# Optimization experiments

Hardware: AMD Instinct MI355X
Metric: run time of the kernel (lower is better)

Reference implementation:

```python
import jax, jax.numpy as jnp
import numpy as np


def _normalize(x):
    # channel mean-subtract then channel L2 normalize, as in MIDMs.forward
    x = x - x.mean(axis=1, keepdims=True)
    return x / jnp.linalg.norm(x, axis=1, keepdims=True)


def setup_inputs() -> dict:
    key = jax.random.key(0)
    ks = jax.random.split(key, 6)
    B, C, H, W = 2, 256, 64, 64
    return {
        "trg_out": jax.random.normal(ks[0], (B, C, H, W), jnp.float32),
        "src_out": jax.random.normal(ks[1], (B, C, H, W), jnp.float32),
        "ref_out": jax.random.normal(ks[2], (B, C, H, W), jnp.float32),
        "src_feats": jax.random.normal(ks[3], (B, 4, H, W), jnp.float32),
        "ref_feats": jax.random.normal(ks[4], (B, 4, H, W), jnp.float32),
        "ref_semantics": jax.random.uniform(ks[5], (B, 151, H, W), jnp.float32),
    }


def reference(trg_out, src_out, ref_out, src_feats, ref_feats, ref_semantics):
    B, C, H, W = trg_out.shape
    L = H * W
    # normalized matching features, flattened over spatial positions
    t = _normalize(trg_out).reshape(B, C, L)   # [B, C, Lt]
    s = _normalize(src_out).reshape(B, C, L)   # [B, C, Ls]
    r = _normalize(ref_out).reshape(B, C, L)

    # Correlation.correlation: dense cosine affinity between all position pairs
    corr_src = jnp.einsum("bci,bcj->bij", t, s)  # [B, Lt, Ls]
    corr_ref = jnp.einsum("bci,bcj->bij", t, r)

    # soft_warp: softmax over source positions, attention-weighted gather
    attn_src = jax.nn.softmax(corr_src, axis=-1)
    attn_ref = jax.nn.softmax(corr_ref, axis=-1)

    warped_src_feat = jnp.einsum("bij,bcj->bci", attn_src,
                                 src_feats.reshape(B, -1, L)).reshape(B, -1, H, W)
    warped_ref_feat = jnp.einsum("bij,bcj->bci", attn_ref,
                                 ref_feats.reshape(B, -1, L)).reshape(B, -1, H, W)
    warped_ref_seg = jnp.einsum("bij,bcj->bci", attn_ref,
                                ref_semantics.reshape(B, -1, L)).reshape(B, -1, H, W)
    return warped_src_feat, warped_ref_feat, warped_ref_seg
```

## Files before the change

kernel.cpp:

```cpp
#include <hip/hip_runtime.h>
#include <hip/hip_bf16.h>
#include <cstdint>
#include <cstddef>

typedef unsigned short u16;
typedef __attribute__((ext_vector_type(8))) __bf16 bf16x8;
typedef __attribute__((ext_vector_type(4))) unsigned u32x4;
typedef __attribute__((ext_vector_type(16))) float f32x16;

#define LPOS 4096
#define CDIM 256
#define LDSBUF 13312

#if __has_builtin(__builtin_amdgcn_exp2f)
#define EXP2(x) __builtin_amdgcn_exp2f(x)
#else
#define EXP2(x) exp2f(x)
#endif

#define GLOAD_LDS16(g, l)                                                      \
  __builtin_amdgcn_global_load_lds(                                            \
      (const __attribute__((address_space(1))) void*)(g),                      \
      (__attribute__((address_space(3))) void*)(l), 16, 0, 0)

__device__ __forceinline__ unsigned f2bfbits(float x) {
  union { float f; unsigned u; } v; v.f = x;
  return (v.u + 0x7FFFu + ((v.u >> 16) & 1u)) >> 16;
}
__device__ __forceinline__ unsigned packbf(float a, float b) {
  __hip_bfloat162 h2 = __float22bfloat162_rn(make_float2(a, b));
  return *(unsigned*)&h2;
}

__global__ void norm_fused(const float* __restrict__ t_in,
                           const float* __restrict__ s_in,
                           const float* __restrict__ r_in,
                           u16* __restrict__ qn, u16* __restrict__ ksn,
                           u16* __restrict__ krn) {
  __shared__ float tile[256 * 33];
  __shared__ float sums[256], sqs[256];
  __shared__ float mv[32], ivv[32];
  int idx = blockIdx.x;
  int ab = idx >> 7, lt = idx & 127;
  int arr = ab >> 1, b = ab & 1;
  int l0 = lt * 32;
  const float* inp = (arr == 0 ? t_in : arr == 1 ? s_in : r_in) + (size_t)b * CDIM * LPOS;
  u16* outp = (arr == 0 ? qn : arr == 1 ? ksn : krn) + (size_t)b * LPOS * CDIM;
  float scale = (arr == 0) ? 1.4426950408889634f : 1.0f;
  int t = threadIdx.x;
  int cg = t >> 5, l = t & 31;
  float sum = 0.f, sq = 0.f;
#pragma unroll 8
  for (int cc = 0; cc < 32; ++cc) {
    int c = cg * 32 + cc;
    float v = inp[(size_t)c * LPOS + l0 + l];
    tile[c * 33 + l] = v;
    sum += v; sq += v * v;
  }
  sums[t] = sum; sqs[t] = sq;
  __syncthreads();
  if (t < 32) {
    float s = 0.f, q = 0.f;
#pragma unroll
    for (int g = 0; g < 8; ++g) { s += sums[g * 32 + t]; q += sqs[g * 32 + t]; }
    float mean = s * (1.0f / CDIM);
    float nsq = q - s * s * (1.0f / CDIM);
    mv[t] = mean;
    ivv[t] = rsqrtf(fmaxf(nsq, 1e-20f)) * scale;
  }
  __syncthreads();
  int c2 = t & 127, ph = t >> 7;
#pragma unroll 4
  for (int rr = 0; rr < 16; ++rr) {
    int pos = ph + rr * 2;
    float m = mv[pos], iv = ivv[pos];
    float v0 = (tile[(2 * c2) * 33 + pos] - m) * iv;
    float v1 = (tile[(2 * c2 + 1) * 33 + pos] - m) * iv;
    *(unsigned*)&outp[(size_t)(l0 + pos) * CDIM + 2 * c2] = packbf(v0, v1);
  }
}

__global__ void build_v(const float* __restrict__ sf, const float* __restrict__ rf,
                        const float* __restrict__ sem,
                        u16* __restrict__ vs, u16* __restrict__ vr) {
  int t = blockIdx.x * 256 + threadIdx.x;
  const int NVS = 2 * 32 * 4096;
  if (t < NVS) {
    int b = t >> 17;
    int c = (t >> 12) & 31;
    int j = t & 4095;
    float v = (c < 4) ? sf[((size_t)b * 4 + c) * LPOS + j] : (c == 4 ? 1.0f : 0.0f);
    vs[t] = (u16)f2bfbits(v);
  } else {
    int t2 = t - NVS;
    if (t2 < 2 * 160 * 4096) {
      int b = t2 / (160 * 4096);
      int rr = t2 % (160 * 4096);
      int c = rr >> 12, j = rr & 4095;
      float v = (c < 151) ? sem[((size_t)b * 151 + c) * LPOS + j]
              : (c < 155) ? rf[((size_t)b * 4 + (c - 151)) * LPOS + j]
              : (c == 155) ? 1.0f : 0.0f;
      vr[((size_t)b * 160 + c) * LPOS + j] = (u16)f2bfbits(v);
    }
  }
}

template <int CT>
__device__ __forceinline__ void flash_body(
    const u16* __restrict__ qb, const u16* __restrict__ kb,
    const u16* __restrict__ vb, float* __restrict__ dst,
    u16 (*lds)[LDSBUF], int wave, int lane, int i_wave, int j_base, int iters) {
  int h = lane >> 5, ln = lane & 31;

  bf16x8 qf[16];
  const u16* qrow = qb + (size_t)(i_wave + ln) * CDIM;
#pragma unroll
  for (int kt = 0; kt < 16; ++kt)
    qf[kt] = *(const bf16x8*)(qrow + kt * 16 + h * 8);
#pragma unroll
  for (int kt = 0; kt < 16; ++kt)
    asm volatile("" : "+v"(*(u32x4*)&qf[kt]));

  f32x16 O[CT];
#pragma unroll
  for (int c = 0; c < CT; ++c)
#pragma unroll
    for (int t = 0; t < 16; ++t) O[c][t] = 0.0f;

  auto stage = [&](int j0s, int buf) {
#pragma unroll
    for (int g = 0; g < 4; ++g) {
      int G = wave * 4 + g;
      int j = 2 * G + h;
      GLOAD_LDS16(kb + (size_t)(j0s + j) * CDIM + (ln ^ (j & 7)) * 8,
                  &lds[buf][G * 512]);
    }
    if constexpr (CT == 5) {
#pragma unroll
      for (int g = 0; g < 3; ++g) {
        int s = wave * 3 + g;
        if (s < 10) {
          int f = s * 64 + lane;
          int p = f / 160;
          int c = f - p * 160;
          GLOAD_LDS16(vb + (size_t)c * LPOS + j0s + p * 8,
                      &lds[buf][8192 + s * 512]);
        }
      }
    }
  };

  int kread_base = ln * 256 + 8 * (h ^ (ln & 1));
  int q = (ln >> 1) & 3;
  const u16* ka[4];
#pragma unroll
  for (int m = 0; m < 4; ++m) ka[m] = &lds[0][kread_base + 16 * (m ^ q)];
  const u16* va = &lds[0][8192 + h * 1280 + ln * 8];

  auto iter_body = [&](int jt, int buf) {
    int j0 = j_base + jt * 32;
    int bo = buf * LDSBUF;
    __syncthreads();

    bf16x8 vf[2];
    if constexpr (CT == 1) {
#pragma unroll
      for (int kt2 = 0; kt2 < 2; ++kt2)
        vf[kt2] = *(const bf16x8*)(vb + (size_t)ln * LPOS + j0 + (2 * kt2 + h) * 8);
    }
    if (jt + 1 < iters) stage(j0 + 32, buf ^ 1);
    f32x16 Sa, Sb;
#pragma unroll
    for (int t = 0; t < 16; ++t) { Sa[t] = 0.0f; Sb[t] = 0.0f; }
#pragma unroll
    for (int kt = 0; kt < 16; kt += 2) {
      bf16x8 ka0 = *(const bf16x8*)(ka[kt & 3] + 64 * (kt >> 2) + bo);
      Sa = __builtin_amdgcn_mfma_f32_32x32x16_bf16(ka0, qf[kt], Sa, 0, 0, 0);
      bf16x8 ka1 = *(const bf16x8*)(ka[(kt + 1) & 3] + 64 * ((kt + 1) >> 2) + bo);
      Sb = __builtin_amdgcn_mfma_f32_32x32x16_bf16(ka1, qf[kt + 1], Sb, 0, 0, 0);
    }
    f32x16 S;
#pragma unroll
    for (int t = 0; t < 16; ++t) S[t] = EXP2(Sa[t] + Sb[t]);

    bf16x8 pb[2];
#pragma unroll
    for (int kh = 0; kh < 2; ++kh) {
      unsigned c0 = packbf(S[kh * 8 + 0], S[kh * 8 + 1]);
      unsigned c1 = packbf(S[kh * 8 + 2], S[kh * 8 + 3]);
      unsigned c2 = packbf(S[kh * 8 + 4], S[kh * 8 + 5]);
      unsigned c3 = packbf(S[kh * 8 + 6], S[kh * 8 + 7]);
      unsigned keep0 = h ? c2 : c0, keep1 = h ? c3 : c1;
      unsigned send0 = h ? c0 : c2, send1 = h ? c1 : c3;
      unsigned recv0 = (unsigned)__shfl_xor((int)send0, 32, 64);
      unsigned recv1 = (unsigned)__shfl_xor((int)send1, 32, 64);
      union { unsigned u[4]; bf16x8 v; } tmp;
      tmp.u[0] = h ? recv0 : keep0;
      tmp.u[1] = h ? recv1 : keep1;
      tmp.u[2] = h ? keep0 : recv0;
      tmp.u[3] = h ? keep1 : recv1;
      pb[kh] = tmp.v;
    }

#pragma unroll
    for (int ct = 0; ct < CT; ++ct)
#pragma unroll
      for (int kt2 = 0; kt2 < 2; ++kt2) {
        bf16x8 vax;
        if constexpr (CT == 5)
          vax = *(const bf16x8*)(va + kt2 * 2560 + ct * 256 + bo);
        else
          vax = vf[kt2];
        O[ct] = __builtin_amdgcn_mfma_f32_32x32x16_bf16(vax, pb[kt2], O[ct], 0, 0, 0);
      }
  };

  stage(j_base, 0);
  for (int jt = 0; jt < iters; jt += 2) {
    iter_body(jt, 0);
    iter_body(jt + 1, 1);
  }

#pragma unroll
  for (int ct = 0; ct < CT; ++ct)
#pragma unroll
    for (int t = 0; t < 16; ++t) {
      int c = ct * 32 + (t & 3) + 8 * (t >> 2) + 4 * h;
      dst[(size_t)c * LPOS + i_wave + ln] = O[ct][t];
    }
}

__global__ __launch_bounds__(256, 2) void flash(
    const u16* __restrict__ qn, const u16* __restrict__ ksn, const u16* __restrict__ krn,
    const u16* __restrict__ vs, const u16* __restrict__ vr,
    float* __restrict__ nsrc, float* __restrict__ nref,
    int nch_src, int nch_ref) {
  __shared__ u16 lds[2][LDSBUF];
  int tid = threadIdx.x;
  int wave = tid >> 6, lane = tid & 63;
  int idx = blockIdx.x;
  int third = idx / 3, m = idx - third * 3;
  if (m == 0) {
    int r = third;
    int chunk = r >> 6, b = (r >> 5) & 1, wgi = r & 31;
    int jchunk = LPOS / nch_ref;
    flash_body<5>(qn + (size_t)b * LPOS * CDIM, krn + (size_t)b * LPOS * CDIM,
                  vr + (size_t)b * 160 * LPOS,
                  nref + (size_t)(chunk * 2 + b) * 160 * LPOS,
                  lds, wave, lane, wgi * 128 + wave * 32, chunk * jchunk,
                  jchunk / 32);
  } else {
    int r = idx - third - 1;
    int chunk = r >> 6, b = (r >> 5) & 1, wgi = r & 31;
    int jchunk = LPOS / nch_src;
    flash_body<1>(qn + (size_t)b * LPOS * CDIM, ksn + (size_t)b * LPOS * CDIM,
                  vs + (size_t)b * 32 * LPOS,
                  nsrc + (size_t)(chunk * 2 + b) * 32 * LPOS,
                  lds, wave, lane, wgi * 128 + wave * 32, chunk * jchunk,
                  jchunk / 32);
  }
}

__global__ void finalize(const float* __restrict__ nsrc, const float* __restrict__ nref,
                         float* __restrict__ out, int nch_src, int nch_ref) {
  int t = blockIdx.x * 256 + threadIdx.x;
  if (t >= 1302528) return;
  if (t < 32768) {
    int b = t >> 14, c = (t >> 12) & 3, i = t & 4095;
    float num = 0.f, den = 0.f;
    for (int k = 0; k < nch_src; ++k) {
      const float* base = nsrc + ((size_t)(k * 2 + b) * 32) * LPOS;
      num += base[(size_t)c * LPOS + i];
      den += base[(size_t)4 * LPOS + i];
    }
    out[t] = num / den;
  } else if (t < 65536) {
    int t1 = t - 32768;
    int b = t1 >> 14, c = (t1 >> 12) & 3, i = t1 & 4095;
    float num = 0.f, den = 0.f;
    for (int k = 0; k < nch_ref; ++k) {
      const float* base = nref + ((size_t)(k * 2 + b) * 160) * LPOS;
      num += base[(size_t)(151 + c) * LPOS + i];
      den += base[(size_t)155 * LPOS + i];
    }
    out[t] = num / den;
  } else {
    int t2 = t - 65536;
    int b = t2 / 618496;
    int rr = t2 % 618496;
    int c = rr >> 12, i = rr & 4095;
    float num = 0.f, den = 0.f;
    for (int k = 0; k < nch_ref; ++k) {
      const float* base = nref + ((size_t)(k * 2 + b) * 160) * LPOS;
      num += base[(size_t)c * LPOS + i];
      den += base[(size_t)155 * LPOS + i];
    }
    out[t] = num / den;
  }
}

extern "C" void kernel_launch(void* const* d_in, const int* in_sizes, int n_in,
                              void* d_out, int out_size, void* d_ws, size_t ws_size,
                              hipStream_t stream) {
  const float* trg  = (const float*)d_in[0];
  const float* srcp = (const float*)d_in[1];
  const float* refp = (const float*)d_in[2];
  const float* sfeat = (const float*)d_in[3];
  const float* rfeat = (const float*)d_in[4];
  const float* rsem  = (const float*)d_in[5];
  float* out = (float*)d_out;

  char* ws = (char*)d_ws;
  size_t o = 0;
  auto alloc = [&](size_t bytes) -> char* {
    char* p = ws + o;
    o += (bytes + 255) & ~(size_t)255;
    return p;
  };
  u16* qn  = (u16*)alloc(2ull * LPOS * CDIM * 2);
  u16* ksn = (u16*)alloc(2ull * LPOS * CDIM * 2);
  u16* krn = (u16*)alloc(2ull * LPOS * CDIM * 2);
  u16* vs  = (u16*)alloc(2ull * 32 * LPOS * 2);
  u16* vr  = (u16*)alloc(2ull * 160 * LPOS * 2);

  size_t fixed = o;
  int nch_ref = 8;
  for (;;) {
    size_t need = fixed + 512 +
                  (size_t)(2 * nch_ref) * 2 * 32 * LPOS * 4 +
                  (size_t)nch_ref * 2 * 160 * LPOS * 4;
    if (need <= ws_size || nch_ref == 1) break;
    nch_ref >>= 1;
  }
  int nch_src = 2 * nch_ref;
  float* nsrc = (float*)alloc((size_t)nch_src * 2 * 32 * LPOS * 4);
  float* nref = (float*)alloc((size_t)nch_ref * 2 * 160 * LPOS * 4);

  hipLaunchKernelGGL(norm_fused, dim3(768), dim3(256), 0, stream,
                     trg, srcp, refp, qn, ksn, krn);
  hipLaunchKernelGGL(build_v, dim3(6144), dim3(256), 0, stream,
                     sfeat, rfeat, rsem, vs, vr);
  hipLaunchKernelGGL(flash, dim3(64 * nch_ref * 3), dim3(256), 0, stream,
                     qn, ksn, krn, vs, vr, nsrc, nref, nch_src, nch_ref);
  hipLaunchKernelGGL(finalize, dim3(5088), dim3(256), 0, stream,
                     nsrc, nref, out, nch_src, nch_ref);
}
```

Before: 168.5 us.

## Double key tile per iteration and read V directly from blocked global layout

Each flash iteration now processes 64 key positions instead of 32, staging only K tiles into a larger LDS buffer and reading V fragments straight from global memory. To make those loads contiguous, build_v writes V in a blocked [j/8][channel][8] layout. The src and ref paths now use the same chunk count, interleaved one-to-one in the grid instead of one ref block per two src blocks. This is meant to halve barrier and loop overhead and drop V staging through LDS. The cost is more register pressure, LDS use rising from about 52 KB to 64 KB per block, and possible load imbalance because ref blocks do five times the P·V work of src blocks.

```diff
diff --git a/kernel.cpp b/kernel.cpp
--- a/kernel.cpp
+++ b/kernel.cpp
@@ -5,12 +5,10 @@
 
 typedef unsigned short u16;
 typedef __attribute__((ext_vector_type(8))) __bf16 bf16x8;
-typedef __attribute__((ext_vector_type(4))) unsigned u32x4;
 typedef __attribute__((ext_vector_type(16))) float f32x16;
 
 #define LPOS 4096
 #define CDIM 256
-#define LDSBUF 13312
 
 #if __has_builtin(__builtin_amdgcn_exp2f)
 #define EXP2(x) __builtin_amdgcn_exp2f(x)
@@ -90,7 +88,7 @@
     int c = (t >> 12) & 31;
     int j = t & 4095;
     float v = (c < 4) ? sf[((size_t)b * 4 + c) * LPOS + j] : (c == 4 ? 1.0f : 0.0f);
-    vs[t] = (u16)f2bfbits(v);
+    vs[(((size_t)b * 512 + (j >> 3)) * 32 + c) * 8 + (j & 7)] = (u16)f2bfbits(v);
   } else {
     int t2 = t - NVS;
     if (t2 < 2 * 160 * 4096) {
@@ -100,7 +98,7 @@
       float v = (c < 151) ? sem[((size_t)b * 151 + c) * LPOS + j]
               : (c < 155) ? rf[((size_t)b * 4 + (c - 151)) * LPOS + j]
               : (c == 155) ? 1.0f : 0.0f;
-      vr[((size_t)b * 160 + c) * LPOS + j] = (u16)f2bfbits(v);
+      vr[(((size_t)b * 512 + (j >> 3)) * 160 + c) * 8 + (j & 7)] = (u16)f2bfbits(v);
     }
   }
 }
@@ -109,17 +107,15 @@
 __device__ __forceinline__ void flash_body(
     const u16* __restrict__ qb, const u16* __restrict__ kb,
     const u16* __restrict__ vb, float* __restrict__ dst,
-    u16 (*lds)[LDSBUF], int wave, int lane, int i_wave, int j_base, int iters) {
+    u16 (*lds)[16384], int wave, int lane, int i_wave, int j_base, int iters) {
   int h = lane >> 5, ln = lane & 31;
+  const int CV = CT * 32;
 
   bf16x8 qf[16];
   const u16* qrow = qb + (size_t)(i_wave + ln) * CDIM;
 #pragma unroll
   for (int kt = 0; kt < 16; ++kt)
     qf[kt] = *(const bf16x8*)(qrow + kt * 16 + h * 8);
-#pragma unroll
-  for (int kt = 0; kt < 16; ++kt)
-    asm volatile("" : "+v"(*(u32x4*)&qf[kt]));
 
   f32x16 O[CT];
 #pragma unroll
@@ -129,63 +125,68 @@
 
   auto stage = [&](int j0s, int buf) {
 #pragma unroll
-    for (int g = 0; g < 4; ++g) {
-      int G = wave * 4 + g;
+    for (int g = 0; g < 8; ++g) {
+      int G = wave * 8 + g;
       int j = 2 * G + h;
       GLOAD_LDS16(kb + (size_t)(j0s + j) * CDIM + (ln ^ (j & 7)) * 8,
                   &lds[buf][G * 512]);
     }
-    if constexpr (CT == 5) {
-#pragma unroll
-      for (int g = 0; g < 3; ++g) {
-        int s = wave * 3 + g;
-        if (s < 10) {
-          int f = s * 64 + lane;
-          int p = f / 160;
-          int c = f - p * 160;
-          GLOAD_LDS16(vb + (size_t)c * LPOS + j0s + p * 8,
-                      &lds[buf][8192 + s * 512]);
-        }
-      }
-    }
   };
 
   int kread_base = ln * 256 + 8 * (h ^ (ln & 1));
   int q = (ln >> 1) & 3;
-  const u16* ka[4];
-#pragma unroll
-  for (int m = 0; m < 4; ++m) ka[m] = &lds[0][kread_base + 16 * (m ^ q)];
-  const u16* va = &lds[0][8192 + h * 1280 + ln * 8];
+
+  stage(j_base, 0);
 
   auto iter_body = [&](int jt, int buf) {
-    int j0 = j_base + jt * 32;
-    int bo = buf * LDSBUF;
+    int j0 = j_base + jt * 64;
+    int o0 = j0 >> 3;
+    int bo = buf * 16384;
     __syncthreads();
 
-    bf16x8 vf[2];
+    bf16x8 vfA[2][CT], vfB[2][CT];
+#pragma unroll
+    for (int k2 = 0; k2 < 2; ++k2)
+#pragma unroll
+      for (int ct = 0; ct < CT; ++ct)
+        vfA[k2][ct] = *(const bf16x8*)(vb +
+            ((size_t)(o0 + 2 * k2 + h) * CV + ct * 32 + ln) * 8);
     if constexpr (CT == 1) {
 #pragma unroll
-      for (int kt2 = 0; kt2 < 2; ++kt2)
-        vf[kt2] = *(const bf16x8*)(vb + (size_t)ln * LPOS + j0 + (2 * kt2 + h) * 8);
-    }
-    if (jt + 1 < iters) stage(j0 + 32, buf ^ 1);
-    f32x16 Sa, Sb;
-#pragma unroll
-    for (int t = 0; t < 16; ++t) { Sa[t] = 0.0f; Sb[t] = 0.0f; }
-#pragma unroll
-    for (int kt = 0; kt < 16; kt += 2) {
-      bf16x8 ka0 = *(const bf16x8*)(ka[kt & 3] + 64 * (kt >> 2) + bo);
-      Sa = __builtin_amdgcn_mfma_f32_32x32x16_bf16(ka0, qf[kt], Sa, 0, 0, 0);
-      bf16x8 ka1 = *(const bf16x8*)(ka[(kt + 1) & 3] + 64 * ((kt + 1) >> 2) + bo);
-      Sb = __builtin_amdgcn_mfma_f32_32x32x16_bf16(ka1, qf[kt + 1], Sb, 0, 0, 0);
-    }
-    f32x16 S;
-#pragma unroll
-    for (int t = 0; t < 16; ++t) S[t] = EXP2(Sa[t] + Sb[t]);
-
-    bf16x8 pb[2];
-#pragma unroll
-    for (int kh = 0; kh < 2; ++kh) {
+      for (int k2 = 0; k2 < 2; ++k2)
+        vfB[k2][0] = *(const bf16x8*)(vb +
+            ((size_t)(o0 + 2 * k2 + 4 + h) * CV + ln) * 8);
+    }
+    if (jt + 1 < iters) stage(j0 + 64, buf ^ 1);
+
+    f32x16 S0, S1;
+#pragma unroll
+    for (int t = 0; t < 16; ++t) { S0[t] = 0.0f; S1[t] = 0.0f; }
+#pragma unroll
+    for (int kt = 0; kt < 16; ++kt) {
+      int ko = kread_base + 16 * ((kt & 3) ^ q) + 64 * (kt >> 2) + bo;
+      bf16x8 a0 = *(const bf16x8*)&lds[0][ko];
+      S0 = __builtin_amdgcn_mfma_f32_32x32x16_bf16(a0, qf[kt], S0, 0, 0, 0);
+      bf16x8 a1 = *(const bf16x8*)&lds[0][ko + 8192];
+      S1 = __builtin_amdgcn_mfma_f32_32x32x16_bf16(a1, qf[kt], S1, 0, 0, 0);
+    }
+    if constexpr (CT == 5) {
+#pragma unroll
+      for (int k2 = 0; k2 < 2; ++k2)
+#pragma unroll
+        for (int ct = 0; ct < CT; ++ct)
+          vfB[k2][ct] = *(const bf16x8*)(vb +
+              ((size_t)(o0 + 2 * k2 + 4 + h) * CV + ct * 32 + ln) * 8);
+    }
+
+#pragma unroll
+    for (int t = 0; t < 16; ++t) { S0[t] = EXP2(S0[t]); S1[t] = EXP2(S1[t]); }
+
+    bf16x8 pb[4];
+#pragma unroll
+    for (int kt2 = 0; kt2 < 4; ++kt2) {
+      const f32x16& S = (kt2 < 2) ? S0 : S1;
+      int kh = kt2 & 1;
       unsigned c0 = packbf(S[kh * 8 + 0], S[kh * 8 + 1]);
       unsigned c1 = packbf(S[kh * 8 + 2], S[kh * 8 + 3]);
       unsigned c2 = packbf(S[kh * 8 + 4], S[kh * 8 + 5]);
@@ -199,23 +200,18 @@
       tmp.u[1] = h ? recv1 : keep1;
       tmp.u[2] = h ? keep0 : recv0;
       tmp.u[3] = h ? keep1 : recv1;
-      pb[kh] = tmp.v;
-    }
-
-#pragma unroll
-    for (int ct = 0; ct < CT; ++ct)
-#pragma unroll
-      for (int kt2 = 0; kt2 < 2; ++kt2) {
-        bf16x8 vax;
-        if constexpr (CT == 5)
-          vax = *(const bf16x8*)(va + kt2 * 2560 + ct * 256 + bo);
-        else
-          vax = vf[kt2];
-        O[ct] = __builtin_amdgcn_mfma_f32_32x32x16_bf16(vax, pb[kt2], O[ct], 0, 0, 0);
-      }
+      pb[kt2] = tmp.v;
+    }
+
+#pragma unroll
+    for (int ct = 0; ct < CT; ++ct) {
+      O[ct] = __builtin_amdgcn_mfma_f32_32x32x16_bf16(vfA[0][ct], pb[0], O[ct], 0, 0, 0);
+      O[ct] = __builtin_amdgcn_mfma_f32_32x32x16_bf16(vfA[1][ct], pb[1], O[ct], 0, 0, 0);
+      O[ct] = __builtin_amdgcn_mfma_f32_32x32x16_bf16(vfB[0][ct], pb[2], O[ct], 0, 0, 0);
+      O[ct] = __builtin_amdgcn_mfma_f32_32x32x16_bf16(vfB[1][ct], pb[3], O[ct], 0, 0, 0);
+    }
   };
 
-  stage(j_base, 0);
   for (int jt = 0; jt < iters; jt += 2) {
     iter_body(jt, 0);
     iter_body(jt + 1, 1);
@@ -233,42 +229,38 @@
 __global__ __launch_bounds__(256, 2) void flash(
     const u16* __restrict__ qn, const u16* __restrict__ ksn, const u16* __restrict__ krn,
     const u16* __restrict__ vs, const u16* __restrict__ vr,
-    float* __restrict__ nsrc, float* __restrict__ nref,
-    int nch_src, int nch_ref) {
-  __shared__ u16 lds[2][LDSBUF];
+    float* __restrict__ nsrc, float* __restrict__ nref, int nch) {
+  __shared__ u16 lds[2][16384];
   int tid = threadIdx.x;
   int wave = tid >> 6, lane = tid & 63;
   int idx = blockIdx.x;
-  int third = idx / 3, m = idx - third * 3;
-  if (m == 0) {
-    int r = third;
-    int chunk = r >> 6, b = (r >> 5) & 1, wgi = r & 31;
-    int jchunk = LPOS / nch_ref;
-    flash_body<5>(qn + (size_t)b * LPOS * CDIM, krn + (size_t)b * LPOS * CDIM,
-                  vr + (size_t)b * 160 * LPOS,
+  bool is_ref = !(idx & 1);
+  int r = idx >> 1;
+  int chunk = r >> 6, b = (r >> 5) & 1, wgi = r & 31;
+  int jchunk = LPOS / nch;
+  int j_base = chunk * jchunk;
+  int iters = jchunk / 64;
+  int i_wave = wgi * 128 + wave * 32;
+  const u16* qb = qn + (size_t)b * LPOS * CDIM;
+  if (is_ref) {
+    flash_body<5>(qb, krn + (size_t)b * LPOS * CDIM, vr + (size_t)b * 160 * LPOS,
                   nref + (size_t)(chunk * 2 + b) * 160 * LPOS,
-                  lds, wave, lane, wgi * 128 + wave * 32, chunk * jchunk,
-                  jchunk / 32);
+                  lds, wave, lane, i_wave, j_base, iters);
   } else {
-    int r = idx - third - 1;
-    int chunk = r >> 6, b = (r >> 5) & 1, wgi = r & 31;
-    int jchunk = LPOS / nch_src;
-    flash_body<1>(qn + (size_t)b * LPOS * CDIM, ksn + (size_t)b * LPOS * CDIM,
-                  vs + (size_t)b * 32 * LPOS,
+    flash_body<1>(qb, ksn + (size_t)b * LPOS * CDIM, vs + (size_t)b * 32 * LPOS,
                   nsrc + (size_t)(chunk * 2 + b) * 32 * LPOS,
-                  lds, wave, lane, wgi * 128 + wave * 32, chunk * jchunk,
-                  jchunk / 32);
+                  lds, wave, lane, i_wave, j_base, iters);
   }
 }
 
 __global__ void finalize(const float* __restrict__ nsrc, const float* __restrict__ nref,
-                         float* __restrict__ out, int nch_src, int nch_ref) {
+                         float* __restrict__ out, int nch) {
   int t = blockIdx.x * 256 + threadIdx.x;
   if (t >= 1302528) return;
   if (t < 32768) {
     int b = t >> 14, c = (t >> 12) & 3, i = t & 4095;
     float num = 0.f, den = 0.f;
-    for (int k = 0; k < nch_src; ++k) {
+    for (int k = 0; k < nch; ++k) {
       const float* base = nsrc + ((size_t)(k * 2 + b) * 32) * LPOS;
       num += base[(size_t)c * LPOS + i];
       den += base[(size_t)4 * LPOS + i];
@@ -278,7 +270,7 @@
     int t1 = t - 32768;
     int b = t1 >> 14, c = (t1 >> 12) & 3, i = t1 & 4095;
     float num = 0.f, den = 0.f;
-    for (int k = 0; k < nch_ref; ++k) {
+    for (int k = 0; k < nch; ++k) {
       const float* base = nref + ((size_t)(k * 2 + b) * 160) * LPOS;
       num += base[(size_t)(151 + c) * LPOS + i];
       den += base[(size_t)155 * LPOS + i];
@@ -290,7 +282,7 @@
     int rr = t2 % 618496;
     int c = rr >> 12, i = rr & 4095;
     float num = 0.f, den = 0.f;
-    for (int k = 0; k < nch_ref; ++k) {
+    for (int k = 0; k < nch; ++k) {
       const float* base = nref + ((size_t)(k * 2 + b) * 160) * LPOS;
       num += base[(size_t)c * LPOS + i];
       den += base[(size_t)155 * LPOS + i];
@@ -324,24 +316,23 @@
   u16* vr  = (u16*)alloc(2ull * 160 * LPOS * 2);
 
   size_t fixed = o;
-  int nch_ref = 8;
+  int nch = 8;
   for (;;) {
     size_t need = fixed + 512 +
-                  (size_t)(2 * nch_ref) * 2 * 32 * LPOS * 4 +
-                  (size_t)nch_ref * 2 * 160 * LPOS * 4;
-    if (need <= ws_size || nch_ref == 1) break;
-    nch_ref >>= 1;
-  }
-  int nch_src = 2 * nch_ref;
-  float* nsrc = (float*)alloc((size_t)nch_src * 2 * 32 * LPOS * 4);
-  float* nref = (float*)alloc((size_t)nch_ref * 2 * 160 * LPOS * 4);
+                  (size_t)nch * 2 * 32 * LPOS * 4 +
+                  (size_t)nch * 2 * 160 * LPOS * 4;
+    if (need <= ws_size || nch == 2) break;
+    nch >>= 1;
+  }
+  float* nsrc = (float*)alloc((size_t)nch * 2 * 32 * LPOS * 4);
+  float* nref = (float*)alloc((size_t)nch * 2 * 160 * LPOS * 4);
 
   hipLaunchKernelGGL(norm_fused, dim3(768), dim3(256), 0, stream,
                      trg, srcp, refp, qn, ksn, krn);
   hipLaunchKernelGGL(build_v, dim3(6144), dim3(256), 0, stream,
                      sfeat, rfeat, rsem, vs, vr);
-  hipLaunchKernelGGL(flash, dim3(64 * nch_ref * 3), dim3(256), 0, stream,
-                     qn, ksn, krn, vs, vr, nsrc, nref, nch_src, nch_ref);
+  hipLaunchKernelGGL(flash, dim3(128 * nch), dim3(256), 0, stream,
+                     qn, ksn, krn, vs, vr, nsrc, nref, nch);
   hipLaunchKernelGGL(finalize, dim3(5088), dim3(256), 0, stream,
-                     nsrc, nref, out, nch_src, nch_ref);
-}
+                     nsrc, nref, out, nch);
+}
```

New measurement: 183.4 us. 1.09x slower.
